# Performance work log

Hardware: AMD Instinct MI355X
Metric: run time of the kernel (lower is better)

The kernel has to match this reference:

```python
import jax, jax.numpy as jnp
import numpy as np

B, S, D, H = 2, 2048, 1024, 16
HD = D // H  # head dim = 64

def setup_inputs() -> dict:
    key = jax.random.key(0)
    k1, k2, k3, k4, k5 = jax.random.split(key, 5)
    return {
        "x": jax.random.normal(k1, (B, S, D), dtype=jnp.float32),
        "w_qkv": jax.random.normal(k2, (D, 3 * D), dtype=jnp.float32) * (1.0 / np.sqrt(D)),
        "b_qkv": jax.random.normal(k3, (3 * D,), dtype=jnp.float32) * 0.02,
        "w_out": jax.random.normal(k4, (D, D), dtype=jnp.float32) * (1.0 / np.sqrt(D)),
        "b_out": jax.random.normal(k5, (D,), dtype=jnp.float32) * 0.02,
        "c": 0,
    }

def reference(x, w_qkv, b_qkv, w_out, b_out, c):
    # fused QKV projection: [B,S,3D]
    qkv = jnp.einsum('bsd,de->bse', x, w_qkv) + b_qkv
    q, k, v = jnp.split(qkv, 3, axis=-1)
    # [B,S,D] -> [B,H,S,HD]
    split_heads = lambda t: t.reshape(B, S, H, HD).transpose(0, 2, 1, 3)
    q, k, v = split_heads(q), split_heads(k), split_heads(v)
    scale = 1.0 / np.sqrt(HD).astype(np.float32)
    scores = jnp.einsum('bhqd,bhkd->bhqk', q, k) * scale  # [B,H,S,S]
    probs = jax.nn.softmax(scores, axis=-1)
    # c==1 noise path references an undefined `const` in the original (dead/broken);
    # dropout probs are 0 -> identity (eval mode).
    attn = jnp.einsum('bhqk,bhkd->bhqd', probs, v)  # [B,H,S,HD]
    attn = attn.transpose(0, 2, 1, 3).reshape(B, S, D)
    out = jnp.einsum('bsd,de->bse', attn, w_out) + b_out
    return out
```

## Files before the change

kernel.cpp:

```cpp
#include <hip/hip_runtime.h>


typedef __attribute__((ext_vector_type(8))) short bs8;
typedef __attribute__((ext_vector_type(4))) short bs4;
typedef __attribute__((ext_vector_type(4))) float f32x4;
typedef __attribute__((ext_vector_type(16))) float f32x16;

#define QSCALE 0.18033688011112042f
#define MBOUND 24.0f

__device__ __forceinline__ unsigned short f2bf(float f) {
  union { float f; unsigned int u; } v; v.f = f;
  return (unsigned short)((v.u + 0x8000u) >> 16);
}

__device__ __forceinline__ unsigned int cvtpk(float a, float b) {
#if defined(__HIP_DEVICE_COMPILE__)
  unsigned int r;
  asm("v_cvt_pk_bf16_f32 %0, %1, %2" : "=v"(r) : "v"(a), "v"(b));
  return r;
#else
  return 0u;
#endif
}

__device__ __forceinline__ void pls32(unsigned int &a, unsigned int &b) {
#if defined(__HIP_DEVICE_COMPILE__)
  asm("v_permlane32_swap_b32 %0, %1" : "+v"(a), "+v"(b));
#endif
}

__device__ __forceinline__ void async16(const unsigned short* g, unsigned short* lds) {
  __builtin_amdgcn_global_load_lds(
      (const __attribute__((address_space(1))) unsigned int*)g,
      (__attribute__((address_space(3))) unsigned int*)lds, 16, 0, 0);
}

__device__ __forceinline__ void stage_rows64(unsigned short* lds, const unsigned short* src,
                                             int ldk, int w, int l) {
#pragma unroll
  for (int i = 0; i < 4; ++i) {
    int row = (w * 4 + i) * 8 + (l >> 3);
    int cg  = (l & 7) ^ (l >> 3);
    async16(src + (size_t)row * ldk + cg * 8, lds + (w * 4 + i) * 512);
  }
}

__device__ __forceinline__ void stage_rows64_8w(unsigned short* lds, const unsigned short* src,
                                                int ldk, int w, int l) {
#pragma unroll
  for (int i = 0; i < 2; ++i) {
    int row = (w * 2 + i) * 8 + (l >> 3);
    int cg  = (l & 7) ^ (l >> 3);
    async16(src + (size_t)row * ldk + cg * 8, lds + (w * 2 + i) * 512);
  }
}

__device__ __forceinline__ void stage_vt_8w(unsigned short* lds, const unsigned short* vtb,
                                            int keyofs, int w, int l) {
#pragma unroll
  for (int i = 0; i < 2; ++i) {
    int row = (w * 2 + i) * 4 + (l >> 4);
    int cg = (l & 15) ^ (row & 15);
    async16(vtb + (size_t)row * 2048 + keyofs + cg * 8, lds + (w * 2 + i) * 512);
  }
}

__device__ __forceinline__ void transpose_cast_body(const float* __restrict__ src,
                                                    unsigned short* __restrict__ dst,
                                                    int R, int C, int bx, int by, int t) {
  __shared__ unsigned short tile[64][73];
  int c0 = bx * 64, r0 = by * 64;
  int rl = t >> 2, cb = (t & 3) * 16;
  const float* p = src + (size_t)(r0 + rl) * C + c0 + cb;
#pragma unroll
  for (int j = 0; j < 16; j += 4) {
    float4 f = *(const float4*)(p + j);
    tile[rl][cb + j + 0] = f2bf(f.x);
    tile[rl][cb + j + 1] = f2bf(f.y);
    tile[rl][cb + j + 2] = f2bf(f.z);
    tile[rl][cb + j + 3] = f2bf(f.w);
  }
  __syncthreads();
  int cl = t >> 2, rb = (t & 3) * 16;
  unsigned short* q = dst + (size_t)(c0 + cl) * R + r0 + rb;
#pragma unroll
  for (int j = 0; j < 16; ++j) q[j] = tile[rb + j][cl];
}

__global__ __launch_bounds__(256) void prep_kernel(const float* __restrict__ x,
                                                   unsigned short* __restrict__ xb,
                                                   const float* __restrict__ w_qkv,
                                                   unsigned short* __restrict__ wt1,
                                                   const float* __restrict__ w_out,
                                                   unsigned short* __restrict__ wt2) {
  int blk = blockIdx.x, t = threadIdx.x;
  if (blk < 2048) {
    int i = (blk * 256 + t) * 8;
    float4 a = *(const float4*)(x + i);
    float4 b = *(const float4*)(x + i + 4);
    union { bs8 v; unsigned short u[8]; } o;
    o.u[0] = f2bf(a.x); o.u[1] = f2bf(a.y); o.u[2] = f2bf(a.z); o.u[3] = f2bf(a.w);
    o.u[4] = f2bf(b.x); o.u[5] = f2bf(b.y); o.u[6] = f2bf(b.z); o.u[7] = f2bf(b.w);
    *(bs8*)(xb + i) = o.v;
  } else if (blk < 2816) {
    int i = blk - 2048;
    transpose_cast_body(w_qkv, wt1, 1024, 3072, i % 48, i / 48, t);
  } else {
    int i = blk - 2816;
    transpose_cast_body(w_out, wt2, 1024, 1024, i % 16, i / 16, t);
  }
}

__global__ __launch_bounds__(256) void gemm_qkv_kernel(const unsigned short* __restrict__ A,
                                                       const unsigned short* __restrict__ Bt,
                                                       const float* __restrict__ bias,
                                                       unsigned short* __restrict__ qo,
                                                       unsigned short* __restrict__ ko,
                                                       unsigned short* __restrict__ vto) {
  __shared__ unsigned short As[128 * 64];
  __shared__ unsigned short Bs[128 * 64];
  int t = threadIdx.x, w = t >> 6, l = t & 63;
  int m16 = l & 15, q = l >> 4;
  int wm = w >> 1, wn = w & 1;
  int bm = blockIdx.y, bn = blockIdx.x;
  bool vsec = (bn >= 16);
  const unsigned short* Abase = A + (size_t)bm * 128 * 1024;
  const unsigned short* Bbase = Bt + (size_t)bn * 128 * 1024;
  f32x4 zero4 = {0.f, 0.f, 0.f, 0.f};
  f32x4 acc[4][4];
#pragma unroll
  for (int i = 0; i < 4; ++i)
#pragma unroll
    for (int j = 0; j < 4; ++j) acc[i][j] = zero4;
  for (int kt = 0; kt < 16; ++kt) {
    stage_rows64(As, Abase + kt * 64, 1024, w, l);
    stage_rows64(Bs, Bbase + kt * 64, 1024, w, l);
    __syncthreads();
#pragma unroll
    for (int ks = 0; ks < 2; ++ks) {
      bs8 af[4], bf[4];
#pragma unroll
      for (int mt = 0; mt < 4; ++mt) {
        int row = wm * 64 + mt * 16 + m16;
        int c = ks * 4 + q;
        af[mt] = *(const bs8*)&As[row * 64 + ((c ^ (row & 7)) * 8)];
      }
#pragma unroll
      for (int nt = 0; nt < 4; ++nt) {
        int row = wn * 64 + nt * 16 + m16;
        int c = ks * 4 + q;
        bf[nt] = *(const bs8*)&Bs[row * 64 + ((c ^ (row & 7)) * 8)];
      }
      if (vsec) {
#pragma unroll
        for (int mt = 0; mt < 4; ++mt)
#pragma unroll
          for (int nt = 0; nt < 4; ++nt)
            acc[mt][nt] = __builtin_amdgcn_mfma_f32_16x16x32_bf16(af[mt], bf[nt],
                                                                  acc[mt][nt], 0, 0, 0);
      } else {
#pragma unroll
        for (int mt = 0; mt < 4; ++mt)
#pragma unroll
          for (int nt = 0; nt < 4; ++nt)
            acc[mt][nt] = __builtin_amdgcn_mfma_f32_16x16x32_bf16(bf[nt], af[mt],
                                                                  acc[mt][nt], 0, 0, 0);
      }
    }
    __syncthreads();
  }
  if (!vsec) {
#pragma unroll
    for (int nt = 0; nt < 4; ++nt) {
      int ng0 = bn * 128 + wn * 64 + nt * 16 + q * 4;
      float4 bb = *(const float4*)&bias[ng0];
      int sect = ng0 >> 10;
      unsigned short* dst = sect ? ko : qo;
      float sc = sect ? 1.0f : QSCALE;
      int f0 = ng0 & 1023, h = f0 >> 6, hd0 = f0 & 63;
#pragma unroll
      for (int mt = 0; mt < 4; ++mt) {
        int mg = bm * 128 + wm * 64 + mt * 16 + m16;
        int b = mg >> 11, s = mg & 2047;
        union { bs4 v; unsigned short u[4]; } pv;
        pv.u[0] = f2bf((acc[mt][nt][0] + bb.x) * sc);
        pv.u[1] = f2bf((acc[mt][nt][1] + bb.y) * sc);
        pv.u[2] = f2bf((acc[mt][nt][2] + bb.z) * sc);
        pv.u[3] = f2bf((acc[mt][nt][3] + bb.w) * sc);
        *(bs4*)&dst[((size_t)(b * 16 + h) * 2048 + s) * 64 + hd0] = pv.v;
      }
    }
  } else {
#pragma unroll
    for (int nt = 0; nt < 4; ++nt) {
      int ng = bn * 128 + wn * 64 + nt * 16 + m16;
      float bb = bias[ng];
      int f = ng & 1023, h = f >> 6, hd = f & 63;
#pragma unroll
      for (int mt = 0; mt < 4; ++mt) {
        int mg0 = bm * 128 + wm * 64 + mt * 16 + q * 4;
        int b = mg0 >> 11, s0 = mg0 & 2047;
        union { bs4 v; unsigned short u[4]; } pv;
#pragma unroll
        for (int r = 0; r < 4; ++r) pv.u[r] = f2bf(acc[mt][nt][r] + bb);
        *(bs4*)&vto[((size_t)(b * 16 + h) * 64 + hd) * 2048 + s0] = pv.v;
      }
    }
  }
}

__global__ __launch_bounds__(256) void gemm_out_kernel(const unsigned short* __restrict__ A,
                                                       const unsigned short* __restrict__ Bt,
                                                       const float* __restrict__ bias,
                                                       float* __restrict__ out) {
  __shared__ unsigned short As[64 * 64];
  __shared__ unsigned short Bs[128 * 64];
  int t = threadIdx.x, w = t >> 6, l = t & 63;
  int m16 = l & 15, q = l >> 4;
  int wm = w >> 1, wn = w & 1;
  int bm = blockIdx.y, bn = blockIdx.x;
  const unsigned short* Abase = A + (size_t)bm * 64 * 1024;
  const unsigned short* Bbase = Bt + (size_t)bn * 128 * 1024;
  f32x4 zero4 = {0.f, 0.f, 0.f, 0.f};
  f32x4 acc[2][4];
#pragma unroll
  for (int i = 0; i < 2; ++i)
#pragma unroll
    for (int j = 0; j < 4; ++j) acc[i][j] = zero4;
  for (int kt = 0; kt < 16; ++kt) {
    stage_rows64_8w(As, Abase + kt * 64, 1024, w, l);
    stage_rows64(Bs, Bbase + kt * 64, 1024, w, l);
    __syncthreads();
#pragma unroll
    for (int ks = 0; ks < 2; ++ks) {
      bs8 af[2], bf[4];
#pragma unroll
      for (int mt = 0; mt < 2; ++mt) {
        int row = wm * 32 + mt * 16 + m16;
        int c = ks * 4 + q;
        af[mt] = *(const bs8*)&As[row * 64 + ((c ^ (row & 7)) * 8)];
      }
#pragma unroll
      for (int nt = 0; nt < 4; ++nt) {
        int row = wn * 64 + nt * 16 + m16;
        int c = ks * 4 + q;
        bf[nt] = *(const bs8*)&Bs[row * 64 + ((c ^ (row & 7)) * 8)];
      }
#pragma unroll
      for (int mt = 0; mt < 2; ++mt)
#pragma unroll
        for (int nt = 0; nt < 4; ++nt)
          acc[mt][nt] = __builtin_amdgcn_mfma_f32_16x16x32_bf16(bf[nt], af[mt],
                                                                acc[mt][nt], 0, 0, 0);
    }
    __syncthreads();
  }
#pragma unroll
  for (int nt = 0; nt < 4; ++nt) {
    int ng0 = bn * 128 + wn * 64 + nt * 16 + q * 4;
    float4 bb = *(const float4*)&bias[ng0];
#pragma unroll
    for (int mt = 0; mt < 2; ++mt) {
      int mg = bm * 64 + wm * 32 + mt * 16 + m16;
      float4 ov;
      ov.x = acc[mt][nt][0] + bb.x;
      ov.y = acc[mt][nt][1] + bb.y;
      ov.z = acc[mt][nt][2] + bb.z;
      ov.w = acc[mt][nt][3] + bb.w;
      *(float4*)&out[(size_t)mg * 1024 + ng0] = ov;
    }
  }
}

__global__ __launch_bounds__(512, 4) void attn_kernel(const unsigned short* __restrict__ Q,
                                                      const unsigned short* __restrict__ K,
                                                      const unsigned short* __restrict__ Vt,
                                                      unsigned short* __restrict__ Aout) {
  __shared__ unsigned short Ks[2][128 * 64];
  __shared__ unsigned short Vts[2][64 * 128];
  int t = threadIdx.x, w = t >> 6, l = t & 63;
  int c32 = l & 31, lh = l >> 5;
  int wq = w & 3, kh = w >> 2;
  int qt = blockIdx.x, bh = blockIdx.y;
  const unsigned short* qbase = Q + (size_t)bh * 2048 * 64 + (size_t)qt * 128 * 64;
  const unsigned short* kbase = K + (size_t)bh * 2048 * 64;
  const unsigned short* vtbase = Vt + (size_t)bh * 64 * 2048;

  bs8 qf[4];
#pragma unroll
  for (int ks = 0; ks < 4; ++ks)
    qf[ks] = *(const bs8*)(qbase + (size_t)(wq * 32 + c32) * 64 + ks * 16 + lh * 8);

  stage_rows64_8w(&Ks[0][0], kbase, 64, w, l);
  stage_vt_8w(&Vts[0][0], vtbase, 0, w, l);
  __syncthreads();

  f32x16 sAcc[2];
  f32x16 o[2];
  float lsum = 0.f;
#pragma unroll
  for (int r = 0; r < 16; ++r) { o[0][r] = 0.f; o[1][r] = 0.f; }

  for (int kt = 0; kt < 16; ++kt) {
    int buf = kt & 1;
    if (kt < 15) {
      stage_rows64_8w(&Ks[buf ^ 1][0], kbase + (size_t)(kt + 1) * 128 * 64, 64, w, l);
      stage_vt_8w(&Vts[buf ^ 1][0], vtbase, (kt + 1) * 128, w, l);
    }
    const unsigned short* Kb = &Ks[buf][0];
    const unsigned short* Vb = &Vts[buf][0];

#pragma unroll
    for (int tile = 0; tile < 2; ++tile)
#pragma unroll
      for (int r = 0; r < 16; ++r) sAcc[tile][r] = -MBOUND;
#pragma unroll
    for (int ks = 0; ks < 4; ++ks) {
      int row0 = kh * 64 + c32;
      int row1 = row0 + 32;
      int cgr = ks * 2 + lh;
      bs8 kf0 = *(const bs8*)&Kb[row0 * 64 + ((cgr ^ (row0 & 7)) * 8)];
      bs8 kf1 = *(const bs8*)&Kb[row1 * 64 + ((cgr ^ (row1 & 7)) * 8)];
      __builtin_amdgcn_s_setprio(1);
      sAcc[0] = __builtin_amdgcn_mfma_f32_32x32x16_bf16(kf0, qf[ks], sAcc[0], 0, 0, 0);
      sAcc[1] = __builtin_amdgcn_mfma_f32_32x32x16_bf16(kf1, qf[ks], sAcc[1], 0, 0, 0);
      __builtin_amdgcn_s_setprio(0);
    }

#pragma unroll
    for (int tile = 0; tile < 2; ++tile) {
      float rs = 0.f;
      unsigned int wp[8];
#pragma unroll
      for (int ri = 0; ri < 8; ++ri) {
        float p0 = __builtin_amdgcn_exp2f(sAcc[tile][2 * ri]);
        float p1 = __builtin_amdgcn_exp2f(sAcc[tile][2 * ri + 1]);
        rs += p0 + p1;
        wp[ri] = cvtpk(p0, p1);
      }
      lsum += rs;
#pragma unroll
      for (int kp = 0; kp < 2; ++kp) {
        int ks2 = tile * 2 + kp;
        unsigned int W0 = wp[kp * 4 + 0], W2 = wp[kp * 4 + 2];
        unsigned int W1 = wp[kp * 4 + 1], W3 = wp[kp * 4 + 3];
        pls32(W0, W2);
        pls32(W1, W3);
        union { bs8 v; unsigned int u[4]; } pf;
        pf.u[0] = W0; pf.u[1] = W1; pf.u[2] = W2; pf.u[3] = W3;
        __builtin_amdgcn_s_setprio(1);
#pragma unroll
        for (int nh = 0; nh < 2; ++nh) {
          int vrow = nh * 32 + c32;
          int gk = kh * 8 + ks2 * 2 + lh;
          bs8 vf = *(const bs8*)&Vb[vrow * 128 + ((gk ^ (vrow & 15)) * 8)];
          o[nh] = __builtin_amdgcn_mfma_f32_32x32x16_bf16(vf, pf.v, o[nh], 0, 0, 0);
        }
        __builtin_amdgcn_s_setprio(0);
      }
    }
    __syncthreads();
  }

  float* ored = (float*)&Ks[0][0];
  float* lred = (float*)&Vts[1][0];
  unsigned short* ot = &Vts[0][0];
  int b = bh >> 4, hh = bh & 15;
  if (kh == 1) {
#pragma unroll
    for (int nh = 0; nh < 2; ++nh)
#pragma unroll
      for (int c = 0; c < 4; ++c) {
        f32x4 t4 = { o[nh][c * 4 + 0], o[nh][c * 4 + 1],
                     o[nh][c * 4 + 2], o[nh][c * 4 + 3] };
        *(f32x4*)&ored[((nh * 4 + c) * 256 + wq * 64 + l) * 4] = t4;
      }
    lred[wq * 64 + l] = lsum;
  }
  __syncthreads();
  if (kh == 0) {
#pragma unroll
    for (int nh = 0; nh < 2; ++nh)
#pragma unroll
      for (int c = 0; c < 4; ++c) {
        f32x4 part = *(const f32x4*)&ored[((nh * 4 + c) * 256 + wq * 64 + l) * 4];
#pragma unroll
        for (int r = 0; r < 4; ++r) o[nh][c * 4 + r] += part[r];
      }
    lsum += lred[wq * 64 + l];

    float l0 = lsum;
    l0 += __shfl_xor(l0, 32);
    float inv = 1.0f / l0;

    int token = wq * 32 + c32;
#pragma unroll
    for (int nh = 0; nh < 2; ++nh)
#pragma unroll
      for (int rg = 0; rg < 4; ++rg) {
        union { bs4 v; unsigned int u[2]; } pv;
        pv.u[0] = cvtpk(o[nh][rg * 4 + 0] * inv, o[nh][rg * 4 + 1] * inv);
        pv.u[1] = cvtpk(o[nh][rg * 4 + 2] * inv, o[nh][rg * 4 + 3] * inv);
        int g = nh * 4 + rg;
        *(bs4*)&ot[token * 64 + ((g ^ (token & 7)) * 8) + lh * 4] = pv.v;
      }
  }
  __syncthreads();
#pragma unroll
  for (int ps = 0; ps < 2; ++ps) {
    int idx = ps * 512 + t;
    int token = idx >> 3, g = idx & 7;
    bs8 val = *(const bs8*)&ot[token * 64 + ((g ^ (token & 7)) * 8)];
    *(bs8*)&Aout[((size_t)(b * 2048 + qt * 128 + token)) * 1024 + hh * 64 + g * 8] = val;
  }
}

extern "C" void kernel_launch(void* const* d_in, const int* in_sizes, int n_in,
                              void* d_out, int out_size, void* d_ws, size_t ws_size,
                              hipStream_t stream) {
  const float* x     = (const float*)d_in[0];
  const float* w_qkv = (const float*)d_in[1];
  const float* b_qkv = (const float*)d_in[2];
  const float* w_out = (const float*)d_in[3];
  const float* b_out = (const float*)d_in[4];
  float* out = (float*)d_out;

  char* ws = (char*)d_ws;
  unsigned short* xb    = (unsigned short*)(ws);
  unsigned short* wt1   = (unsigned short*)(ws + (8u << 20));
  unsigned short* wt2   = (unsigned short*)(ws + (14u << 20));
  unsigned short* qb    = (unsigned short*)(ws + (16u << 20));
  unsigned short* kb    = (unsigned short*)(ws + (24u << 20));
  unsigned short* vtb   = (unsigned short*)(ws + (32u << 20));
  unsigned short* attnb = (unsigned short*)(ws + (40u << 20));

  prep_kernel<<<3072, 256, 0, stream>>>(x, xb, w_qkv, wt1, w_out, wt2);
  gemm_qkv_kernel<<<dim3(24, 32), 256, 0, stream>>>(xb, wt1, b_qkv, qb, kb, vtb);
  attn_kernel<<<dim3(16, 32), 512, 0, stream>>>(qb, kb, vtb, attnb);
  gemm_out_kernel<<<dim3(8, 64), 256, 0, stream>>>(attnb, wt2, b_out, out);
}
```

Before: 189.3 us.

## Halve attention query tile, split keys four ways, read V directly from global

The attention kernel now handles 64 queries per block instead of 128. It launches twice as many blocks and splits each 128-key tile across four wave groups of 32 keys rather than two of 64. The V tile is no longer staged in LDS; each wave loads its V fragments straight from global memory, which frees LDS and supports a higher occupancy hint. A block-index swizzle groups blocks from the same head, and the final reduction combines four partial outputs in two LDS passes. In exchange, K is re-staged for every smaller query tile, V reads become uncached and unpipelined, and the reduction needs more synchronisation.

```diff
diff --git a/kernel.cpp b/kernel.cpp
--- a/kernel.cpp
+++ b/kernel.cpp
@@ -53,16 +53,6 @@
     int row = (w * 2 + i) * 8 + (l >> 3);
     int cg  = (l & 7) ^ (l >> 3);
     async16(src + (size_t)row * ldk + cg * 8, lds + (w * 2 + i) * 512);
-  }
-}
-
-__device__ __forceinline__ void stage_vt_8w(unsigned short* lds, const unsigned short* vtb,
-                                            int keyofs, int w, int l) {
-#pragma unroll
-  for (int i = 0; i < 2; ++i) {
-    int row = (w * 2 + i) * 4 + (l >> 4);
-    int cg = (l & 15) ^ (row & 15);
-    async16(vtb + (size_t)row * 2048 + keyofs + cg * 8, lds + (w * 2 + i) * 512);
   }
 }
 
@@ -273,17 +263,18 @@
   }
 }
 
-__global__ __launch_bounds__(512, 4) void attn_kernel(const unsigned short* __restrict__ Q,
+__global__ __launch_bounds__(512, 6) void attn_kernel(const unsigned short* __restrict__ Q,
                                                       const unsigned short* __restrict__ K,
                                                       const unsigned short* __restrict__ Vt,
                                                       unsigned short* __restrict__ Aout) {
   __shared__ unsigned short Ks[2][128 * 64];
-  __shared__ unsigned short Vts[2][64 * 128];
   int t = threadIdx.x, w = t >> 6, l = t & 63;
   int c32 = l & 31, lh = l >> 5;
-  int wq = w & 3, kh = w >> 2;
-  int qt = blockIdx.x, bh = blockIdx.y;
-  const unsigned short* qbase = Q + (size_t)bh * 2048 * 64 + (size_t)qt * 128 * 64;
+  int wq = w & 1, kh = w >> 1;
+  int lid = blockIdx.y * 32 + blockIdx.x;
+  int swz = (lid & 7) * 128 + (lid >> 3);
+  int qt = swz & 31, bh = swz >> 5;
+  const unsigned short* qbase = Q + (size_t)bh * 2048 * 64 + (size_t)qt * 64 * 64;
   const unsigned short* kbase = K + (size_t)bh * 2048 * 64;
   const unsigned short* vtbase = Vt + (size_t)bh * 64 * 2048;
 
@@ -293,107 +284,101 @@
     qf[ks] = *(const bs8*)(qbase + (size_t)(wq * 32 + c32) * 64 + ks * 16 + lh * 8);
 
   stage_rows64_8w(&Ks[0][0], kbase, 64, w, l);
-  stage_vt_8w(&Vts[0][0], vtbase, 0, w, l);
   __syncthreads();
 
-  f32x16 sAcc[2];
+  f32x16 sAcc;
   f32x16 o[2];
   float lsum = 0.f;
 #pragma unroll
   for (int r = 0; r < 16; ++r) { o[0][r] = 0.f; o[1][r] = 0.f; }
 
+  int krow = kh * 32 + c32;
   for (int kt = 0; kt < 16; ++kt) {
     int buf = kt & 1;
-    if (kt < 15) {
+    if (kt < 15)
       stage_rows64_8w(&Ks[buf ^ 1][0], kbase + (size_t)(kt + 1) * 128 * 64, 64, w, l);
-      stage_vt_8w(&Vts[buf ^ 1][0], vtbase, (kt + 1) * 128, w, l);
-    }
     const unsigned short* Kb = &Ks[buf][0];
-    const unsigned short* Vb = &Vts[buf][0];
-
-#pragma unroll
-    for (int tile = 0; tile < 2; ++tile)
-#pragma unroll
-      for (int r = 0; r < 16; ++r) sAcc[tile][r] = -MBOUND;
+
+#pragma unroll
+    for (int r = 0; r < 16; ++r) sAcc[r] = -MBOUND;
 #pragma unroll
     for (int ks = 0; ks < 4; ++ks) {
-      int row0 = kh * 64 + c32;
-      int row1 = row0 + 32;
       int cgr = ks * 2 + lh;
-      bs8 kf0 = *(const bs8*)&Kb[row0 * 64 + ((cgr ^ (row0 & 7)) * 8)];
-      bs8 kf1 = *(const bs8*)&Kb[row1 * 64 + ((cgr ^ (row1 & 7)) * 8)];
+      bs8 kf = *(const bs8*)&Kb[krow * 64 + ((cgr ^ (krow & 7)) * 8)];
       __builtin_amdgcn_s_setprio(1);
-      sAcc[0] = __builtin_amdgcn_mfma_f32_32x32x16_bf16(kf0, qf[ks], sAcc[0], 0, 0, 0);
-      sAcc[1] = __builtin_amdgcn_mfma_f32_32x32x16_bf16(kf1, qf[ks], sAcc[1], 0, 0, 0);
+      sAcc = __builtin_amdgcn_mfma_f32_32x32x16_bf16(kf, qf[ks], sAcc, 0, 0, 0);
       __builtin_amdgcn_s_setprio(0);
     }
 
-#pragma unroll
-    for (int tile = 0; tile < 2; ++tile) {
-      float rs = 0.f;
-      unsigned int wp[8];
-#pragma unroll
-      for (int ri = 0; ri < 8; ++ri) {
-        float p0 = __builtin_amdgcn_exp2f(sAcc[tile][2 * ri]);
-        float p1 = __builtin_amdgcn_exp2f(sAcc[tile][2 * ri + 1]);
-        rs += p0 + p1;
-        wp[ri] = cvtpk(p0, p1);
-      }
-      lsum += rs;
-#pragma unroll
-      for (int kp = 0; kp < 2; ++kp) {
-        int ks2 = tile * 2 + kp;
-        unsigned int W0 = wp[kp * 4 + 0], W2 = wp[kp * 4 + 2];
-        unsigned int W1 = wp[kp * 4 + 1], W3 = wp[kp * 4 + 3];
-        pls32(W0, W2);
-        pls32(W1, W3);
-        union { bs8 v; unsigned int u[4]; } pf;
-        pf.u[0] = W0; pf.u[1] = W1; pf.u[2] = W2; pf.u[3] = W3;
-        __builtin_amdgcn_s_setprio(1);
-#pragma unroll
-        for (int nh = 0; nh < 2; ++nh) {
-          int vrow = nh * 32 + c32;
-          int gk = kh * 8 + ks2 * 2 + lh;
-          bs8 vf = *(const bs8*)&Vb[vrow * 128 + ((gk ^ (vrow & 15)) * 8)];
-          o[nh] = __builtin_amdgcn_mfma_f32_32x32x16_bf16(vf, pf.v, o[nh], 0, 0, 0);
-        }
-        __builtin_amdgcn_s_setprio(0);
-      }
-    }
-    __syncthreads();
-  }
-
-  float* ored = (float*)&Ks[0][0];
-  float* lred = (float*)&Vts[1][0];
-  unsigned short* ot = &Vts[0][0];
-  int b = bh >> 4, hh = bh & 15;
-  if (kh == 1) {
-#pragma unroll
-    for (int nh = 0; nh < 2; ++nh)
+    float rs = 0.f;
+    unsigned int wp[8];
+#pragma unroll
+    for (int ri = 0; ri < 8; ++ri) {
+      float p0 = __builtin_amdgcn_exp2f(sAcc[2 * ri]);
+      float p1 = __builtin_amdgcn_exp2f(sAcc[2 * ri + 1]);
+      rs += p0 + p1;
+      wp[ri] = cvtpk(p0, p1);
+    }
+    lsum += rs;
+
+#pragma unroll
+    for (int kp = 0; kp < 2; ++kp) {
+      unsigned int W0 = wp[kp * 4 + 0], W2 = wp[kp * 4 + 2];
+      unsigned int W1 = wp[kp * 4 + 1], W3 = wp[kp * 4 + 3];
+      pls32(W0, W2);
+      pls32(W1, W3);
+      union { bs8 v; unsigned int u[4]; } pf;
+      pf.u[0] = W0; pf.u[1] = W1; pf.u[2] = W2; pf.u[3] = W3;
+      __builtin_amdgcn_s_setprio(1);
+#pragma unroll
+      for (int nh = 0; nh < 2; ++nh) {
+        const unsigned short* vp = vtbase + (size_t)(nh * 32 + c32) * 2048 +
+                                   kt * 128 + kh * 32 + kp * 16 + lh * 8;
+        bs8 vf = *(const bs8*)vp;
+        o[nh] = __builtin_amdgcn_mfma_f32_32x32x16_bf16(vf, pf.v, o[nh], 0, 0, 0);
+      }
+      __builtin_amdgcn_s_setprio(0);
+    }
+    __syncthreads();
+  }
+
+  float* fs = (float*)&Ks[0][0];
+  int slot = wq * 64 + l;
+#pragma unroll
+  for (int nh = 0; nh < 2; ++nh) {
+    if (kh != 0) {
+      int base = (kh - 1) * 2048 + slot * 16;
 #pragma unroll
       for (int c = 0; c < 4; ++c) {
         f32x4 t4 = { o[nh][c * 4 + 0], o[nh][c * 4 + 1],
                      o[nh][c * 4 + 2], o[nh][c * 4 + 3] };
-        *(f32x4*)&ored[((nh * 4 + c) * 256 + wq * 64 + l) * 4] = t4;
-      }
-    lred[wq * 64 + l] = lsum;
-  }
-  __syncthreads();
+        *(f32x4*)&fs[base + c * 4] = t4;
+      }
+      if (nh == 0) fs[6144 + (kh - 1) * 128 + slot] = lsum;
+    }
+    __syncthreads();
+    if (kh == 0) {
+#pragma unroll
+      for (int kk = 1; kk < 4; ++kk) {
+        int base = (kk - 1) * 2048 + slot * 16;
+#pragma unroll
+        for (int c = 0; c < 4; ++c) {
+          f32x4 part = *(const f32x4*)&fs[base + c * 4];
+#pragma unroll
+          for (int r = 0; r < 4; ++r) o[nh][c * 4 + r] += part[r];
+        }
+        if (nh == 0) lsum += fs[6144 + (kk - 1) * 128 + slot];
+      }
+    }
+    __syncthreads();
+  }
+
+  unsigned short* ot = &Ks[0][0];
+  int b = bh >> 4, hh = bh & 15;
   if (kh == 0) {
-#pragma unroll
-    for (int nh = 0; nh < 2; ++nh)
-#pragma unroll
-      for (int c = 0; c < 4; ++c) {
-        f32x4 part = *(const f32x4*)&ored[((nh * 4 + c) * 256 + wq * 64 + l) * 4];
-#pragma unroll
-        for (int r = 0; r < 4; ++r) o[nh][c * 4 + r] += part[r];
-      }
-    lsum += lred[wq * 64 + l];
-
     float l0 = lsum;
     l0 += __shfl_xor(l0, 32);
     float inv = 1.0f / l0;
-
     int token = wq * 32 + c32;
 #pragma unroll
     for (int nh = 0; nh < 2; ++nh)
@@ -407,12 +392,10 @@
       }
   }
   __syncthreads();
-#pragma unroll
-  for (int ps = 0; ps < 2; ++ps) {
-    int idx = ps * 512 + t;
-    int token = idx >> 3, g = idx & 7;
+  {
+    int token = t >> 3, g = t & 7;
     bs8 val = *(const bs8*)&ot[token * 64 + ((g ^ (token & 7)) * 8)];
-    *(bs8*)&Aout[((size_t)(b * 2048 + qt * 128 + token)) * 1024 + hh * 64 + g * 8] = val;
+    *(bs8*)&Aout[((size_t)(b * 2048 + qt * 64 + token)) * 1024 + hh * 64 + g * 8] = val;
   }
 }
 
@@ -437,6 +420,6 @@
 
   prep_kernel<<<3072, 256, 0, stream>>>(x, xb, w_qkv, wt1, w_out, wt2);
   gemm_qkv_kernel<<<dim3(24, 32), 256, 0, stream>>>(xb, wt1, b_qkv, qb, kb, vtb);
-  attn_kernel<<<dim3(16, 32), 512, 0, stream>>>(qb, kb, vtb, attnb);
+  attn_kernel<<<dim3(32, 32), 512, 0, stream>>>(qb, kb, vtb, attnb);
   gemm_out_kernel<<<dim3(8, 64), 256, 0, stream>>>(attnb, wt2, b_out, out);
 }
```

New measurement: 444.8 us. +135.0%, slower.
